# Optimization experiments

Hardware: AMD Instinct MI355X
Metric: run time of the kernel (lower is better)

## Reference

```python
import jax, jax.numpy as jnp
import numpy as np

B, OBS, ACT, NT, E = 4096, 512, 64, 10, 16
DREP, DH, DK = 1024, 1024, 512  # rep dim, expert hidden, key/value dim


def setup_inputs() -> dict:
    key = jax.random.key(0)
    ks = jax.random.split(key, 24)
    s = 0.02
    state_core = jax.random.normal(ks[0], (B, OBS), jnp.float32)
    task_ids = jax.random.randint(ks[1], (B,), 0, NT)
    onehot = jax.nn.one_hot(task_ids, NT, dtype=jnp.float32)
    state = jnp.concatenate([state_core, onehot], axis=-1)  # [B, OBS+NT]
    act = jax.random.normal(ks[2], (B, ACT), jnp.float32)
    return {
        "state": state,
        "act": act,
        "rep_W0": s * jax.random.normal(ks[3], (OBS + ACT, DREP), jnp.float32),
        "rep_b0": jnp.zeros((DREP,), jnp.float32),
        "rep_W1": s * jax.random.normal(ks[4], (DREP, DREP), jnp.float32),
        "rep_b1": jnp.zeros((DREP,), jnp.float32),
        "emb": 0.5 * jnp.ones((NT, DK), jnp.float32),
        "Wk0": s * jax.random.normal(ks[5], (E, DREP, DH), jnp.float32),
        "bk0": jnp.zeros((E, DH), jnp.float32),
        "Wk1": s * jax.random.normal(ks[6], (E, DH, DK), jnp.float32),
        "bk1": jnp.zeros((E, DK), jnp.float32),
        "Wv0": s * jax.random.normal(ks[7], (E, DREP, DH), jnp.float32),
        "bv0": jnp.zeros((E, DH), jnp.float32),
        "Wv1": s * jax.random.normal(ks[8], (E, DH, DK), jnp.float32),
        "bv1": jnp.zeros((E, DK), jnp.float32),
        "Wt0": s * jax.random.normal(ks[9], (DK, 512), jnp.float32),
        "bt0": jnp.zeros((512,), jnp.float32),
        "Wt1": s * jax.random.normal(ks[10], (512, 256), jnp.float32),
        "bt1": jnp.zeros((256,), jnp.float32),
        "Wt2": s * jax.random.normal(ks[11], (256, 1), jnp.float32),
        "bt2": jnp.zeros((1,), jnp.float32),
    }


def reference(state, act, rep_W0, rep_b0, rep_W1, rep_b1, emb,
              Wk0, bk0, Wk1, bk1, Wv0, bv0, Wv1, bv1,
              Wt0, bt0, Wt1, bt1, Wt2, bt2):
    num_tasks = emb.shape[0]
    task = jnp.argmax(state[:, -num_tasks:], axis=-1)  # one-hot -> index (== torch.nonzero)
    s = state[:, :-num_tasks]
    # representation: mlp([obs+act, 1024, 1024]) -> relu then identity
    x = jnp.concatenate([s, act], axis=-1)
    rep = jax.nn.relu(x @ rep_W0 + rep_b0) @ rep_W1 + rep_b1  # [B, DREP]
    query = jnp.tanh(emb[task])  # [B, DK]
    # all experts batched (original loops in Python over E tiny MLPs)
    hk = jax.nn.relu(jnp.einsum('bd,edh->ebh', rep, Wk0) + bk0[:, None, :])
    keys = jnp.einsum('ebh,ehk->ebk', hk, Wk1) + bk1[:, None, :]   # [E,B,DK]
    hv = jax.nn.relu(jnp.einsum('bd,edh->ebh', rep, Wv0) + bv0[:, None, :])
    vals = jnp.einsum('ebh,ehk->ebk', hv, Wv1) + bv1[:, None, :]   # [E,B,DK]
    logits = jnp.einsum('bk,ebk->be', query, keys)                 # [B,E]
    attn = jax.nn.softmax(logits, axis=1)
    tower_in = jnp.einsum('be,ebk->bk', attn, vals)                # [B,DK]
    h = jax.nn.relu(tower_in @ Wt0 + bt0)
    h = jax.nn.relu(h @ Wt1 + bt1)
    q = jnp.squeeze(h @ Wt2 + bt2, -1)                             # [B]
    expert_loss = -jnp.mean(
        jnp.sum(jnp.clip(jnp.log(attn + 1e-10), -6.0, 0.0), axis=-1) * 0.3)
    return q, expert_loss
```

## Files before the change

kernel.cpp:

```cpp
#include <hip/hip_runtime.h>
#include <cstdint>
#include <cstddef>

#define NB   4096
#define OBS  512
#define NACT 64
#define NT   10
#define NE   16
#define DREP 1024
#define DH   1024
#define DK   512
#define SLD  (OBS + NT)
#define XK   (OBS + NACT)

typedef short s8v __attribute__((ext_vector_type(8)));
typedef float f4v __attribute__((ext_vector_type(4)));

__device__ __forceinline__ unsigned short f2bf(float f) {
  union { float f; unsigned int u; } v; v.f = f;
  unsigned int u = v.u;
  unsigned int r = (u + 0x7FFFu + ((u >> 16) & 1u)) >> 16;
  return (unsigned short)r;
}
__device__ __forceinline__ float bf2f(unsigned short h) {
  union { unsigned int u; float f; } v; v.u = ((unsigned int)h) << 16;
  return v.f;
}

__device__ __forceinline__ void gload_lds16(const unsigned short* gp, const unsigned short* lp) {
  __builtin_amdgcn_global_load_lds(
      (const __attribute__((address_space(1))) void*)(uintptr_t)gp,
      (__attribute__((address_space(3))) void*)(unsigned int)(uintptr_t)lp,
      16, 0, 0);
}

template <int BM, int BN, int MODE, int RELU, int LDA, int LDB, int KK>
__global__ void __launch_bounds__(256)
gemm_k(const unsigned short* __restrict__ A,
       const unsigned short* __restrict__ Bt,
       const float* __restrict__ bias,
       unsigned short* __restrict__ outB, int ldo,
       const float* __restrict__ qk1, const int* __restrict__ task,
       float* __restrict__ logits, int eBase,
       const float* __restrict__ attn, float* __restrict__ cio)
{
  constexpr int FM = BM / 32;
  constexpr int FN = BN / 32;
  constexpr int CA = BM / 64;
  constexpr int CB = BN / 64;
  constexpr int NTILES = KK / 32;
  static_assert((NTILES & 1) == 0, "K-loop unrolled by 2");

  __shared__ __align__(16) unsigned short As[2][BM * 32];
  __shared__ __align__(16) unsigned short Bs[2][BN * 32];

  const int tid  = threadIdx.x;
  const int wave = tid >> 6;
  const int lane = tid & 63;
  const int wm = wave >> 1, wn = wave & 1;

  const int rowBase = blockIdx.x * BM;
  const int colBase = blockIdx.y * BN;

  int eg = 0;
  if (MODE == 1) {
    eg = blockIdx.z;
    Bt  += (size_t)eg * (DREP * DH);
    bias += eg * DH;
    qk1 += (size_t)eg * (NT * DH);
  }
  if (MODE == 2) {
    eg = eBase + blockIdx.z;
    Bt  += (size_t)eg * (DREP * DH);
    bias += eg * DH;
    outB += (size_t)blockIdx.z * DH;
  }
  if (MODE == 3 || MODE == 4) {
    A   += (size_t)blockIdx.z * KK;
    Bt  += (size_t)blockIdx.z * KK;
    cio += (size_t)blockIdx.z * NB * DK;
  }

  f4v acc[FM][FN];
#pragma unroll
  for (int m = 0; m < FM; ++m)
#pragma unroll
    for (int n = 0; n < FN; ++n) acc[m][n] = f4v{0.f, 0.f, 0.f, 0.f};

  const int sRow = lane >> 2;
  const int sSw  = ((lane & 3) ^ ((sRow >> 1) & 3)) * 8;

  const unsigned short* ag[CA];
  const unsigned short* bg[CB];
#pragma unroll
  for (int j = 0; j < CA; ++j)
    ag[j] = A + (size_t)(rowBase + (wave * CA + j) * 16 + sRow) * LDA + sSw;
#pragma unroll
  for (int j = 0; j < CB; ++j)
    bg[j] = Bt + (size_t)(colBase + (wave * CB + j) * 16 + sRow) * LDB + sSw;

  unsigned short* asl[2][CA];
  unsigned short* bsl[2][CB];
#pragma unroll
  for (int b = 0; b < 2; ++b) {
#pragma unroll
    for (int j = 0; j < CA; ++j) asl[b][j] = &As[b][(wave * CA + j) * 512];
#pragma unroll
    for (int j = 0; j < CB; ++j) bsl[b][j] = &Bs[b][(wave * CB + j) * 512];
  }

  const int fr   = lane & 15;
  const int koSw = ((lane >> 4) ^ ((fr >> 1) & 3)) * 8;
  const unsigned short* aRd[2] = { &As[0][(wm * (BM / 2) + fr) * 32 + koSw],
                                   &As[1][(wm * (BM / 2) + fr) * 32 + koSw] };
  const unsigned short* bRd[2] = { &Bs[0][(wn * (BN / 2) + fr) * 32 + koSw],
                                   &Bs[1][(wn * (BN / 2) + fr) * 32 + koSw] };

  auto stage = [&](int buf) {
#pragma unroll
    for (int j = 0; j < CA; ++j) { gload_lds16(ag[j], asl[buf][j]); ag[j] += 32; }
#pragma unroll
    for (int j = 0; j < CB; ++j) { gload_lds16(bg[j], bsl[buf][j]); bg[j] += 32; }
  };

  auto compute = [&](int buf) {
    s8v av[FM], bv[FN];
#pragma unroll
    for (int m = 0; m < FM; ++m)
      av[m] = *reinterpret_cast<const s8v*>(aRd[buf] + m * 512);
#pragma unroll
    for (int n = 0; n < FN; ++n)
      bv[n] = *reinterpret_cast<const s8v*>(bRd[buf] + n * 512);
#pragma unroll
    for (int m = 0; m < FM; ++m)
#pragma unroll
      for (int n = 0; n < FN; ++n)
        acc[m][n] = __builtin_amdgcn_mfma_f32_16x16x32_bf16(av[m], bv[n], acc[m][n], 0, 0, 0);
  };

  stage(0);

  for (int t = 0; t < NTILES; t += 2) {
    __builtin_amdgcn_s_waitcnt(0);
    __builtin_amdgcn_s_barrier();
    if (t + 1 < NTILES) stage(1);
    compute(0);

    __builtin_amdgcn_s_waitcnt(0);
    __builtin_amdgcn_s_barrier();
    if (t + 2 < NTILES) stage(0);
    compute(1);
  }

  const int cr = (lane >> 4) * 4;
  const int cc = lane & 15;

  int gcn[FN];
  float bcol[FN];
#pragma unroll
  for (int n = 0; n < FN; ++n) {
    gcn[n] = colBase + wn * (BN / 2) + n * 16 + cc;
    bcol[n] = (MODE >= 3) ? 0.f : bias[gcn[n]];
  }

  if (MODE == 0 || MODE == 2) {
#pragma unroll
    for (int m = 0; m < FM; ++m)
#pragma unroll
      for (int r = 0; r < 4; ++r) {
        int gr = rowBase + wm * (BM / 2) + m * 16 + cr + r;
        float aw = 1.f;
        if (MODE == 2) aw = attn[gr * NE + eg];
#pragma unroll
        for (int n = 0; n < FN; ++n) {
          float v = acc[m][n][r] + bcol[n];
          if (RELU) v = fmaxf(v, 0.f);
          if (MODE == 2) v *= aw;
          outB[(size_t)gr * ldo + gcn[n]] = f2bf(v);
        }
      }
  }

  if (MODE == 1) {
#pragma unroll
    for (int m = 0; m < FM; ++m)
#pragma unroll
      for (int r = 0; r < 4; ++r) {
        int gr = rowBase + wm * (BM / 2) + m * 16 + cr + r;
        int tk = task[gr];
        const float* qrow = qk1 + (size_t)tk * DH;
        float s = 0.f;
#pragma unroll
        for (int n = 0; n < FN; ++n) {
          float v = fmaxf(acc[m][n][r] + bcol[n], 0.f);
          s += v * qrow[gcn[n]];
        }
#pragma unroll
        for (int off = 1; off < 16; off <<= 1) s += __shfl_xor(s, off, 64);
        if (cc == 0) atomicAdd(&logits[gr * NE + eg], s);
      }
  }

  if (MODE == 3 || MODE == 4) {
#pragma unroll
    for (int m = 0; m < FM; ++m)
#pragma unroll
      for (int r = 0; r < 4; ++r) {
        int gr = rowBase + wm * (BM / 2) + m * 16 + cr + r;
#pragma unroll
        for (int n = 0; n < FN; ++n) {
          float v = acc[m][n][r];
          if (MODE == 4) v += cio[(size_t)gr * DK + gcn[n]];
          cio[(size_t)gr * DK + gcn[n]] = v;
        }
      }
  }
}

__global__ void task_k(const float* __restrict__ state, int* __restrict__ task) {
  int b = blockIdx.x * blockDim.x + threadIdx.x;
  if (b >= NB) return;
  const float* p = state + (size_t)b * SLD + OBS;
  float best = p[0]; int bi = 0;
  for (int j = 1; j < NT; ++j) { float v = p[j]; if (v > best) { best = v; bi = j; } }
  task[b] = bi;
}

__global__ void buildx_k(const float* __restrict__ state, const float* __restrict__ act,
                         unsigned short* __restrict__ x) {
  int idx = blockIdx.x * blockDim.x + threadIdx.x;
  if (idx >= NB * XK) return;
  int b = idx / XK, j = idx - b * XK;
  float v = (j < OBS) ? state[(size_t)b * SLD + j] : act[(size_t)b * NACT + (j - OBS)];
  x[idx] = f2bf(v);
}

__global__ void prep_emb_k(const float* __restrict__ emb, const float* __restrict__ bk1,
                           float* __restrict__ Qt, float* __restrict__ qb) {
  int t = blockIdx.x;
  __shared__ float qsh[DK];
  for (int k = threadIdx.x; k < DK; k += 256) {
    float v = tanhf(emb[t * DK + k]);
    Qt[t * DK + k] = v;
    qsh[k] = v;
  }
  __syncthreads();
  int wave = threadIdx.x >> 6, lane = threadIdx.x & 63;
  for (int e = wave; e < NE; e += 4) {
    float s = 0.f;
    for (int k = lane; k < DK; k += 64) s += qsh[k] * bk1[e * DK + k];
    for (int off = 1; off < 64; off <<= 1) s += __shfl_xor(s, off, 64);
    if (lane == 0) qb[e * NT + t] = s;
  }
}

__global__ void qk1_k(const float* __restrict__ Wk1, const float* __restrict__ Qt,
                      float* __restrict__ qk1) {
  int w = (blockIdx.x * blockDim.x + threadIdx.x) >> 6;
  int lane = threadIdx.x & 63;
  if (w >= NE * DH) return;
  int e = w >> 10, h = w & (DH - 1);
  const float* wrow = Wk1 + ((size_t)e * DH + h) * DK + lane * 8;
  float wv[8];
#pragma unroll
  for (int j = 0; j < 8; ++j) wv[j] = wrow[j];
#pragma unroll
  for (int t = 0; t < NT; ++t) {
    const float* qrow = Qt + t * DK + lane * 8;
    float s = 0.f;
#pragma unroll
    for (int j = 0; j < 8; ++j) s += wv[j] * qrow[j];
#pragma unroll
    for (int off = 1; off < 64; off <<= 1) s += __shfl_xor(s, off, 64);
    if (lane == 0) qk1[((size_t)e * NT + t) * DH + h] = s;
  }
}

__global__ void __launch_bounds__(256)
convT_k(const float* __restrict__ src, unsigned short* __restrict__ dst,
        int N, long sBS, long dBS, int dLd) {
  __shared__ float tile[64][65];
  int e = blockIdx.z;
  int n0 = blockIdx.x * 64, k0 = blockIdx.y * 64;
  src += (size_t)e * sBS + (size_t)k0 * N + n0;
  dst += (size_t)e * dBS + (size_t)n0 * dLd + k0;
  int t = threadIdx.x;
  int c4 = t & 15, kr = t >> 4;
#pragma unroll
  for (int i = 0; i < 4; ++i) {
    float4 v = *(const float4*)(src + (size_t)(kr + i * 16) * N + c4 * 4);
    tile[kr + i * 16][c4 * 4 + 0] = v.x;
    tile[kr + i * 16][c4 * 4 + 1] = v.y;
    tile[kr + i * 16][c4 * 4 + 2] = v.z;
    tile[kr + i * 16][c4 * 4 + 3] = v.w;
  }
  __syncthreads();
  int sub = t & 7, nl = t >> 3;
#pragma unroll
  for (int pass = 0; pass < 2; ++pass) {
    int n = nl + pass * 32;
    unsigned short v8[8];
#pragma unroll
    for (int j = 0; j < 8; ++j) v8[j] = f2bf(tile[sub * 8 + j][n]);
    *reinterpret_cast<s8v*>(dst + (size_t)n * dLd + sub * 8) =
        *reinterpret_cast<const s8v*>(v8);
  }
}

__global__ void softmax_k(const float* __restrict__ logits, const float* __restrict__ qb,
                          const int* __restrict__ task, float* __restrict__ attn,
                          float* __restrict__ lossOut) {
  int b = blockIdx.x * blockDim.x + threadIdx.x;
  int t = task[b];
  float l[NE];
  float mx = -1e30f;
#pragma unroll
  for (int e = 0; e < NE; ++e) { l[e] = logits[b * NE + e] + qb[e * NT + t]; mx = fmaxf(mx, l[e]); }
  float s = 0.f;
#pragma unroll
  for (int e = 0; e < NE; ++e) { l[e] = expf(l[e] - mx); s += l[e]; }
  float inv = 1.f / s;
  float loss = 0.f;
#pragma unroll
  for (int e = 0; e < NE; ++e) {
    float a = l[e] * inv;
    attn[b * NE + e] = a;
    float lg = logf(a + 1e-10f);
    loss += fminf(fmaxf(lg, -6.f), 0.f);
  }
  for (int off = 1; off < 64; off <<= 1) loss += __shfl_xor(loss, off, 64);
  if ((threadIdx.x & 63) == 0) atomicAdd(lossOut, loss * (-0.3f / NB));
}

__global__ void towerbias_k(const float* __restrict__ attn, const float* __restrict__ bv1,
                            float* __restrict__ towerin) {
  int idx = blockIdx.x * blockDim.x + threadIdx.x;
  if (idx >= NB * DK) return;
  int b = idx >> 9, k = idx & (DK - 1);
  float s = 0.f;
#pragma unroll
  for (int e = 0; e < NE; ++e) s += attn[b * NE + e] * bv1[e * DK + k];
  towerin[idx] = s;
}

__global__ void cvt_ti_k(const float* __restrict__ twin, const float* __restrict__ P,
                         unsigned short* __restrict__ ti) {
  int idx = (blockIdx.x * blockDim.x + threadIdx.x) * 8;
  if (idx >= NB * DK) return;
  float v[8];
#pragma unroll
  for (int j = 0; j < 8; ++j) v[j] = twin[idx + j];
#pragma unroll
  for (int c = 0; c < 4; ++c) {
    const float* p = P + (size_t)c * NB * DK + idx;
#pragma unroll
    for (int j = 0; j < 8; ++j) v[j] += p[j];
  }
  unsigned short v8[8];
#pragma unroll
  for (int j = 0; j < 8; ++j) v8[j] = f2bf(v[j]);
  *reinterpret_cast<s8v*>(ti + idx) = *reinterpret_cast<const s8v*>(v8);
}

__global__ void qfinal_k(const unsigned short* __restrict__ h2, const float* __restrict__ Wt2,
                         const float* __restrict__ bt2, float* __restrict__ out) {
  int w = (blockIdx.x * blockDim.x + threadIdx.x) >> 6;
  int lane = threadIdx.x & 63;
  if (w >= NB) return;
  float s = 0.f;
#pragma unroll
  for (int j = 0; j < 4; ++j) {
    int k = lane * 4 + j;
    s += bf2f(h2[(size_t)w * 256 + k]) * Wt2[k];
  }
  for (int off = 1; off < 64; off <<= 1) s += __shfl_xor(s, off, 64);
  if (lane == 0) out[w] = s + bt2[0];
}

extern "C" void kernel_launch(void* const* d_in, const int* in_sizes, int n_in,
                              void* d_out, int out_size, void* d_ws, size_t ws_size,
                              hipStream_t stream) {
  const float* state  = (const float*)d_in[0];
  const float* act    = (const float*)d_in[1];
  const float* rep_W0 = (const float*)d_in[2];
  const float* rep_b0 = (const float*)d_in[3];
  const float* rep_W1 = (const float*)d_in[4];
  const float* rep_b1 = (const float*)d_in[5];
  const float* emb    = (const float*)d_in[6];
  const float* Wk0    = (const float*)d_in[7];
  const float* bk0    = (const float*)d_in[8];
  const float* Wk1    = (const float*)d_in[9];
  const float* bk1    = (const float*)d_in[10];
  const float* Wv0    = (const float*)d_in[11];
  const float* bv0    = (const float*)d_in[12];
  const float* Wv1    = (const float*)d_in[13];
  const float* bv1    = (const float*)d_in[14];
  const float* Wt0    = (const float*)d_in[15];
  const float* bt0    = (const float*)d_in[16];
  const float* Wt1    = (const float*)d_in[17];
  const float* bt1    = (const float*)d_in[18];
  const float* Wt2    = (const float*)d_in[19];
  const float* bt2    = (const float*)d_in[20];
  float* out = (float*)d_out;

  char* wsb = (char*)d_ws;
  size_t off = 0;
  auto alloc = [&](size_t bytes) -> void* {
    void* p = wsb + off;
    off += (bytes + 255) & ~(size_t)255;
    return p;
  };
  unsigned short* Ap    = (unsigned short*)alloc((size_t)NB * 8192 * 2);
  unsigned short* Wk0t  = (unsigned short*)alloc((size_t)NE * DREP * DH * 2);
  unsigned short* Wv0t  = (unsigned short*)alloc((size_t)NE * DREP * DH * 2);
  unsigned short* Wv1t  = (unsigned short*)alloc((size_t)DK * (NE * DH) * 2);
  float*          P     = (float*)alloc((size_t)4 * NB * DK * 4);
  unsigned short* h0    = (unsigned short*)alloc((size_t)NB * DREP * 2);
  unsigned short* rep   = (unsigned short*)alloc((size_t)NB * DREP * 2);
  float*          twin  = (float*)alloc((size_t)NB * DK * 4);
  unsigned short* xbuf  = (unsigned short*)alloc((size_t)NB * XK * 2);
  unsigned short* ti    = (unsigned short*)alloc((size_t)NB * DK * 2);
  unsigned short* h1    = (unsigned short*)alloc((size_t)NB * 512 * 2);
  unsigned short* h2    = (unsigned short*)alloc((size_t)NB * 256 * 2);
  unsigned short* rW1t  = (unsigned short*)alloc((size_t)DREP * DREP * 2);
  unsigned short* rW0t  = (unsigned short*)alloc((size_t)DREP * XK * 2);
  float*          qk1   = (float*)alloc((size_t)NE * NT * DH * 4);
  unsigned short* Wt0t  = (unsigned short*)alloc((size_t)512 * 512 * 2);
  unsigned short* Wt1t  = (unsigned short*)alloc((size_t)256 * 512 * 2);
  float*          logits= (float*)alloc((size_t)NB * NE * 4);
  float*          attn  = (float*)alloc((size_t)NB * NE * 4);
  float*          Qt    = (float*)alloc((size_t)NT * DK * 4);
  int*            task  = (int*)alloc((size_t)NB * 4);
  float*          qb    = (float*)alloc((size_t)NE * NT * 4);

  hipMemsetAsync(logits, 0, (size_t)NB * NE * 4, stream);
  hipMemsetAsync(out + NB, 0, sizeof(float), stream);

  task_k<<<NB / 256, 256, 0, stream>>>(state, task);
  buildx_k<<<(NB * XK + 255) / 256, 256, 0, stream>>>(state, act, xbuf);
  prep_emb_k<<<NT, 256, 0, stream>>>(emb, bk1, Qt, qb);
  qk1_k<<<NE * DH / 4, 256, 0, stream>>>(Wk1, Qt, qk1);

  convT_k<<<dim3(DREP / 64, XK / 64, 1), 256, 0, stream>>>(rep_W0, rW0t, DREP, 0, 0, XK);
  convT_k<<<dim3(DREP / 64, DREP / 64, 1), 256, 0, stream>>>(rep_W1, rW1t, DREP, 0, 0, DREP);
  convT_k<<<dim3(DH / 64, DREP / 64, NE), 256, 0, stream>>>(Wk0, Wk0t, DH, (long)DREP * DH, (long)DREP * DH, DREP);
  convT_k<<<dim3(DH / 64, DREP / 64, NE), 256, 0, stream>>>(Wv0, Wv0t, DH, (long)DREP * DH, (long)DREP * DH, DREP);
  convT_k<<<dim3(DK / 64, DH / 64, NE), 256, 0, stream>>>(Wv1, Wv1t, DK, (long)DH * DK, 1024L, NE * DH);
  convT_k<<<dim3(512 / 64, 512 / 64, 1), 256, 0, stream>>>(Wt0, Wt0t, 512, 0, 0, 512);
  convT_k<<<dim3(256 / 64, 512 / 64, 1), 256, 0, stream>>>(Wt1, Wt1t, 256, 0, 0, 512);

  gemm_k<128, 128, 0, 1, XK, XK, XK><<<dim3(NB / 128, DREP / 128, 1), 256, 0, stream>>>(
      xbuf, rW0t, rep_b0, h0, DREP, nullptr, nullptr, nullptr, 0, nullptr, nullptr);
  gemm_k<128, 128, 0, 0, DREP, DREP, DREP><<<dim3(NB / 128, DREP / 128, 1), 256, 0, stream>>>(
      h0, rW1t, rep_b1, rep, DREP, nullptr, nullptr, nullptr, 0, nullptr, nullptr);

  gemm_k<128, 128, 1, 1, DREP, DREP, DREP><<<dim3(NB / 128, DH / 128, NE), 256, 0, stream>>>(
      rep, Wk0t, bk0, nullptr, 0, qk1, task, logits, 0, nullptr, nullptr);

  softmax_k<<<NB / 256, 256, 0, stream>>>(logits, qb, task, attn, out + NB);
  towerbias_k<<<NB * DK / 256, 256, 0, stream>>>(attn, bv1, twin);

  for (int g = 0; g < 2; ++g) {
    gemm_k<128, 128, 2, 1, DREP, DREP, DREP><<<dim3(NB / 128, DH / 128, 8), 256, 0, stream>>>(
        rep, Wv0t, bv0, Ap, 8192, nullptr, nullptr, nullptr, g * 8, attn, nullptr);
    if (g == 0)
      gemm_k<128, 128, 3, 0, 8192, NE * DH, 2048><<<dim3(NB / 128, DK / 128, 4), 256, 0, stream>>>(
          Ap, Wv1t, nullptr, nullptr, 0, nullptr, nullptr, nullptr, 0, nullptr, P);
    else
      gemm_k<128, 128, 4, 0, 8192, NE * DH, 2048><<<dim3(NB / 128, DK / 128, 4), 256, 0, stream>>>(
          Ap, Wv1t + (size_t)8192, nullptr, nullptr, 0, nullptr, nullptr, nullptr, 0, nullptr, P);
  }
  cvt_ti_k<<<(NB * DK / 8 + 255) / 256, 256, 0, stream>>>(twin, P, ti);

  gemm_k<64, 64, 0, 1, DK, DK, DK><<<dim3(NB / 64, 512 / 64, 1), 256, 0, stream>>>(
      ti, Wt0t, bt0, h1, 512, nullptr, nullptr, nullptr, 0, nullptr, nullptr);
  gemm_k<64, 64, 0, 1, 512, 512, 512><<<dim3(NB / 64, 256 / 64, 1), 256, 0, stream>>>(
      h1, Wt1t, bt1, h2, 256, nullptr, nullptr, nullptr, 0, nullptr, nullptr);
  qfinal_k<<<NB / 4, 256, 0, stream>>>(h2, Wt2, bt2, out);
}
```

Before: 838.7 us.

## Triple-buffer GEMM K-loop with partial vmcnt waits

Moves the bf16 MFMA GEMM from a double-buffered to a triple-buffered LDS pipeline with two stages in flight. Each step waits with a vmcnt immediate that leaves the newest stage's loads outstanding, instead of draining everything with waitcnt(0). The goal is to hide global-to-LDS latency behind MFMA work. In exchange it uses 50% more shared memory, which can reduce occupancy, and it depends on a hand-encoded waitcnt immediate.

```diff
diff --git a/kernel.cpp b/kernel.cpp
--- a/kernel.cpp
+++ b/kernel.cpp
@@ -49,10 +49,14 @@
   constexpr int CA = BM / 64;
   constexpr int CB = BN / 64;
   constexpr int NTILES = KK / 32;
-  static_assert((NTILES & 1) == 0, "K-loop unrolled by 2");
-
-  __shared__ __align__(16) unsigned short As[2][BM * 32];
-  __shared__ __align__(16) unsigned short Bs[2][BN * 32];
+  static_assert(NTILES >= 3, "pipeline depth");
+  constexpr int LPS = CA + CB;
+  static_assert(LPS < 16, "vmcnt immediate fits in low bits");
+  constexpr int WAIT_STAGE = 0xF70 | LPS;
+  constexpr int WAIT_ALL   = 0xF70;
+
+  __shared__ __align__(16) unsigned short As[3][BM * 32];
+  __shared__ __align__(16) unsigned short Bs[3][BN * 32];
 
   const int tid  = threadIdx.x;
   const int wave = tid >> 6;
@@ -99,38 +103,26 @@
   for (int j = 0; j < CB; ++j)
     bg[j] = Bt + (size_t)(colBase + (wave * CB + j) * 16 + sRow) * LDB + sSw;
 
-  unsigned short* asl[2][CA];
-  unsigned short* bsl[2][CB];
-#pragma unroll
-  for (int b = 0; b < 2; ++b) {
-#pragma unroll
-    for (int j = 0; j < CA; ++j) asl[b][j] = &As[b][(wave * CA + j) * 512];
-#pragma unroll
-    for (int j = 0; j < CB; ++j) bsl[b][j] = &Bs[b][(wave * CB + j) * 512];
-  }
-
   const int fr   = lane & 15;
   const int koSw = ((lane >> 4) ^ ((fr >> 1) & 3)) * 8;
-  const unsigned short* aRd[2] = { &As[0][(wm * (BM / 2) + fr) * 32 + koSw],
-                                   &As[1][(wm * (BM / 2) + fr) * 32 + koSw] };
-  const unsigned short* bRd[2] = { &Bs[0][(wn * (BN / 2) + fr) * 32 + koSw],
-                                   &Bs[1][(wn * (BN / 2) + fr) * 32 + koSw] };
+  const int aOff = (wm * (BM / 2) + fr) * 32 + koSw;
+  const int bOff = (wn * (BN / 2) + fr) * 32 + koSw;
 
   auto stage = [&](int buf) {
 #pragma unroll
-    for (int j = 0; j < CA; ++j) { gload_lds16(ag[j], asl[buf][j]); ag[j] += 32; }
-#pragma unroll
-    for (int j = 0; j < CB; ++j) { gload_lds16(bg[j], bsl[buf][j]); bg[j] += 32; }
+    for (int j = 0; j < CA; ++j) { gload_lds16(ag[j], &As[buf][(wave * CA + j) * 512]); ag[j] += 32; }
+#pragma unroll
+    for (int j = 0; j < CB; ++j) { gload_lds16(bg[j], &Bs[buf][(wave * CB + j) * 512]); bg[j] += 32; }
   };
 
   auto compute = [&](int buf) {
     s8v av[FM], bv[FN];
 #pragma unroll
     for (int m = 0; m < FM; ++m)
-      av[m] = *reinterpret_cast<const s8v*>(aRd[buf] + m * 512);
+      av[m] = *reinterpret_cast<const s8v*>(&As[buf][aOff + m * 512]);
 #pragma unroll
     for (int n = 0; n < FN; ++n)
-      bv[n] = *reinterpret_cast<const s8v*>(bRd[buf] + n * 512);
+      bv[n] = *reinterpret_cast<const s8v*>(&Bs[buf][bOff + n * 512]);
 #pragma unroll
     for (int m = 0; m < FM; ++m)
 #pragma unroll
@@ -139,17 +131,28 @@
   };
 
   stage(0);
-
-  for (int t = 0; t < NTILES; t += 2) {
-    __builtin_amdgcn_s_waitcnt(0);
+  stage(1);
+
+  for (int t = 0; t < NTILES; t += 3) {
+    if (t + 1 < NTILES) __builtin_amdgcn_s_waitcnt(WAIT_STAGE);
+    else                __builtin_amdgcn_s_waitcnt(WAIT_ALL);
     __builtin_amdgcn_s_barrier();
-    if (t + 1 < NTILES) stage(1);
+    if (t + 2 < NTILES) stage(2);
     compute(0);
-
-    __builtin_amdgcn_s_waitcnt(0);
-    __builtin_amdgcn_s_barrier();
-    if (t + 2 < NTILES) stage(0);
-    compute(1);
+    if (t + 1 < NTILES) {
+      if (t + 2 < NTILES) __builtin_amdgcn_s_waitcnt(WAIT_STAGE);
+      else                __builtin_amdgcn_s_waitcnt(WAIT_ALL);
+      __builtin_amdgcn_s_barrier();
+      if (t + 3 < NTILES) stage(0);
+      compute(1);
+    }
+    if (t + 2 < NTILES) {
+      if (t + 3 < NTILES) __builtin_amdgcn_s_waitcnt(WAIT_STAGE);
+      else                __builtin_amdgcn_s_waitcnt(WAIT_ALL);
+      __builtin_amdgcn_s_barrier();
+      if (t + 4 < NTILES) stage(1);
+      compute(2);
+    }
   }
 
   const int cr = (lane >> 4) * 4;
```

After: 767.8 us. 8.5% less time.
